# Optimization experiments

Measured on AMD Instinct MI355X. Metric: run time of the kernel, lower is better.

The kernel has to match this reference:

```python
import jax, jax.numpy as jnp
import numpy as np

B, N, F = 2, 512, 128
NUM_BASIS = 4


def _mlp(x, W1, b1, W2, b2, W3, b3):
    # two hidden ReLU layers, linear output -> [..., NUM_BASIS]
    h = jax.nn.relu(x @ W1 + b1)
    h = jax.nn.relu(h @ W2 + b2)
    return h @ W3 + b3


def setup_inputs() -> dict:
    key = jax.random.key(0)
    ks = jax.random.split(key, 12)
    s = 0.05  # keep activations O(1)
    inp = {
        "pointwise_features": jax.random.normal(ks[0], (B, N, F), jnp.float32),
        "relative_features": jax.random.normal(ks[1], (B, N, N, F), jnp.float32),
        "pointwise_basis": jax.random.normal(ks[2], (B, N, NUM_BASIS, 3), jnp.float32),
        "relative_basis": jax.random.normal(ks[3], (B, N, N, NUM_BASIS, 3), jnp.float32),
        "pw_W1": jax.random.normal(ks[4], (F, 128), jnp.float32) * s,
        "pw_b1": jnp.zeros((128,), jnp.float32),
        "pw_W2": jax.random.normal(ks[5], (128, 128), jnp.float32) * s,
        "pw_b2": jnp.zeros((128,), jnp.float32),
        "pw_W3": jax.random.normal(ks[6], (128, NUM_BASIS), jnp.float32) * s,
        "pw_b3": jnp.zeros((NUM_BASIS,), jnp.float32),
        "rel_W1": jax.random.normal(ks[7], (F, 128), jnp.float32) * s,
        "rel_b1": jnp.zeros((128,), jnp.float32),
        "rel_W2": jax.random.normal(ks[8], (128, 128), jnp.float32) * s,
        "rel_b2": jnp.zeros((128,), jnp.float32),
        "rel_W3": jax.random.normal(ks[9], (128, NUM_BASIS), jnp.float32) * s,
        "rel_b3": jnp.zeros((NUM_BASIS,), jnp.float32),
        # last 64 atoms are padding (masked) in every batch element
        "masked_elements": jnp.broadcast_to(jnp.arange(N) >= N - 64, (B, N)),
    }
    return inp


def reference(pointwise_features, relative_features, pointwise_basis, relative_basis,
              pw_W1, pw_b1, pw_W2, pw_b2, pw_W3, pw_b3,
              rel_W1, rel_b1, rel_W2, rel_b2, rel_W3, rel_b3,
              masked_elements):
    unmasked = ~masked_elements                      # [B, N]
    num_atoms = unmasked.sum(-1).astype(pointwise_features.dtype)  # [B]

    # pointwise_shift: [B, N, K, 3]
    pw_scale = _mlp(pointwise_features, pw_W1, pw_b1, pw_W2, pw_b2, pw_W3, pw_b3)
    pointwise_shift = pointwise_basis * pw_scale[..., None]

    # relative_shift: [B, N, N, K, 3], mask over j, mean over j
    rel_scale = _mlp(relative_features, rel_W1, rel_b1, rel_W2, rel_b2, rel_W3, rel_b3)
    relative_shift = relative_basis * rel_scale[..., None]
    relative_shift = relative_shift * unmasked[:, None, :, None, None]
    relative_shift = relative_shift.sum(-3) / num_atoms[:, None, None, None]  # [B, N, K, 3]

    all_shifts = pointwise_shift + relative_shift
    shift = all_shifts.sum(-2) / num_atoms[:, None, None]  # [B, N, 3]
    return shift
```

## Files before the change

### kernel.cpp

```cpp
#include <hip/hip_runtime.h>
#include <stdint.h>

#define LDK 136

typedef __attribute__((ext_vector_type(4))) float f32x4;
typedef __attribute__((ext_vector_type(8))) short bf16x8;

__device__ inline unsigned short f2bf_rtne(float f) {
    union { float f; unsigned u; } v; v.f = f;
    unsigned u = v.u;
    u += 0x7fffu + ((u >> 16) & 1u);
    return (unsigned short)(u >> 16);
}

__global__ void prep_kernel(const float* __restrict__ relW1, const float* __restrict__ relW2,
                            const float* __restrict__ pwW1, const float* __restrict__ pwW2,
                            const float* __restrict__ relW3, const float* __restrict__ pwW3,
                            const void* __restrict__ maskp,
                            float* __restrict__ maskf, float* __restrict__ na,
                            unsigned short* __restrict__ w1T_rel, unsigned short* __restrict__ w2T_rel,
                            unsigned short* __restrict__ w1T_pw, unsigned short* __restrict__ w2T_pw,
                            unsigned short* __restrict__ w3T_rel, unsigned short* __restrict__ w3T_pw) {
    int t = threadIdx.x;
    const float* srcs[4] = {relW1, relW2, pwW1, pwW2};
    unsigned short* dsts[4] = {w1T_rel, w2T_rel, w1T_pw, w2T_pw};
    int e0 = blockIdx.x * 1024 + t;
#pragma unroll
    for (int i = 0; i < 4; ++i) {
        int e = e0 + i * 256;
        int mat = e >> 14, o = e & 16383;
        int n = o >> 7, k = o & 127;
        dsts[mat][o] = f2bf_rtne(srcs[mat][k * 128 + n]);
    }
    if (blockIdx.x == 1) {
        for (int i = t; i < 2048; i += 256) {
            int r = i >> 7, h = i & 127;
            w3T_rel[i] = (r < 4) ? f2bf_rtne(relW3[h * 4 + r]) : (unsigned short)0;
            w3T_pw[i]  = (r < 4) ? f2bf_rtne(pwW3[h * 4 + r])  : (unsigned short)0;
        }
    }
    if (blockIdx.x == 0) {
        __shared__ int anyb;
        __shared__ float cnt[2];
        if (t == 0) anyb = 0;
        if (t < 2) cnt[t] = 0.f;
        __syncthreads();
        const unsigned char* mb = (const unsigned char*)maskp;
        int la = 0;
        for (int i = t; i < 1024; i += 256) la |= mb[i];
        if (la) atomicOr(&anyb, 1);
        __syncthreads();
        bool isbyte = (anyb != 0);
        const int* mi = (const int*)maskp;
        float loc0 = 0.f, loc1 = 0.f;
        for (int i = t; i < 1024; i += 256) {
            int v = isbyte ? (int)mb[i] : mi[i];
            float um = (v != 0) ? 0.f : 1.f;
            maskf[i] = um;
            if (i < 512) loc0 += um; else loc1 += um;
        }
        atomicAdd(&cnt[0], loc0);
        atomicAdd(&cnt[1], loc1);
        __syncthreads();
        if (t < 2) na[t] = cnt[t];
    }
}

__global__ __launch_bounds__(256, 2)
void mlp_kernel(const float* __restrict__ X,
                const unsigned short* __restrict__ w1T,
                const unsigned short* __restrict__ w2T,
                const unsigned short* __restrict__ w3T,
                const float* __restrict__ b1, const float* __restrict__ b2,
                const float* __restrict__ b3,
                float* __restrict__ Sout) {
    __shared__ short xs[64 * LDK];
    __shared__ short hs[2][64 * LDK];
    __shared__ float bs1[128], bs2[128], b3s[4];

    int t = threadIdx.x;
    int w = t >> 6, lane = t & 63, q = lane >> 4, col = lane & 15;

    if (t < 128) { bs1[t] = b1[t]; bs2[t] = b2[t]; }
    if (t < 4) b3s[t] = b3[t];

    bf16x8 w1f[2][4], w2f[2][4], w3f[4];
#pragma unroll
    for (int tn = 0; tn < 2; ++tn)
#pragma unroll
        for (int kc = 0; kc < 4; ++kc) {
            int n = w * 32 + tn * 16 + col;
            int kk = kc * 32 + q * 8;
            w1f[tn][kc] = *(const bf16x8*)&w1T[n * 128 + kk];
            w2f[tn][kc] = *(const bf16x8*)&w2T[n * 128 + kk];
        }
#pragma unroll
    for (int kc = 0; kc < 4; ++kc)
        w3f[kc] = *(const bf16x8*)&w3T[col * 128 + kc * 32 + q * 8];

    long rowbase = (long)blockIdx.x * 256;
    int r0 = t >> 5, cg = t & 31;

    float4 px[8];
    {
        const float4* Xg = (const float4*)(X + rowbase * 128);
#pragma unroll
        for (int i = 0; i < 8; ++i) px[i] = Xg[(r0 + 8 * i) * 32 + cg];
#pragma unroll
        for (int i = 0; i < 8; ++i) {
            float4 v = px[i];
            short4 s4 = make_short4((short)f2bf_rtne(v.x), (short)f2bf_rtne(v.y),
                                    (short)f2bf_rtne(v.z), (short)f2bf_rtne(v.w));
            *(short4*)&xs[(r0 + 8 * i) * LDK + cg * 4] = s4;
        }
    }
    __syncthreads();

    for (int tile = 0; tile < 4; ++tile) {
        int hp = tile & 1;
        if (tile < 3) {
            const float4* Xg2 = (const float4*)(X + (rowbase + (long)(tile + 1) * 64) * 128);
#pragma unroll
            for (int i = 0; i < 8; ++i) px[i] = Xg2[(r0 + 8 * i) * 32 + cg];
        }

        f32x4 acc[2][4];
#pragma unroll
        for (int tn = 0; tn < 2; ++tn)
#pragma unroll
            for (int tm = 0; tm < 4; ++tm) acc[tn][tm] = (f32x4)(0.f);
#pragma unroll
        for (int kc = 0; kc < 4; ++kc) {
            bf16x8 bf[4];
#pragma unroll
            for (int tm = 0; tm < 4; ++tm)
                bf[tm] = *(const bf16x8*)&xs[(tm * 16 + col) * LDK + kc * 32 + q * 8];
#pragma unroll
            for (int tn = 0; tn < 2; ++tn)
#pragma unroll
                for (int tm = 0; tm < 4; ++tm)
                    acc[tn][tm] = __builtin_amdgcn_mfma_f32_16x16x32_bf16(w1f[tn][kc], bf[tm], acc[tn][tm], 0, 0, 0);
        }

#pragma unroll
        for (int tn = 0; tn < 2; ++tn)
#pragma unroll
            for (int tm = 0; tm < 4; ++tm) {
                int n0 = w * 32 + tn * 16 + q * 4;
                int m = tm * 16 + col;
                float4 bb = *(const float4*)&bs1[n0];
                short4 s4 = make_short4(
                    (short)f2bf_rtne(fmaxf(acc[tn][tm][0] + bb.x, 0.f)),
                    (short)f2bf_rtne(fmaxf(acc[tn][tm][1] + bb.y, 0.f)),
                    (short)f2bf_rtne(fmaxf(acc[tn][tm][2] + bb.z, 0.f)),
                    (short)f2bf_rtne(fmaxf(acc[tn][tm][3] + bb.w, 0.f)));
                *(short4*)&hs[hp][m * LDK + n0] = s4;
            }
        __syncthreads();

        if (tile < 3) {
#pragma unroll
            for (int i = 0; i < 8; ++i) {
                float4 v = px[i];
                short4 s4 = make_short4((short)f2bf_rtne(v.x), (short)f2bf_rtne(v.y),
                                        (short)f2bf_rtne(v.z), (short)f2bf_rtne(v.w));
                *(short4*)&xs[(r0 + 8 * i) * LDK + cg * 4] = s4;
            }
        }

        f32x4 acc2[2][4];
#pragma unroll
        for (int tn = 0; tn < 2; ++tn)
#pragma unroll
            for (int tm = 0; tm < 4; ++tm) acc2[tn][tm] = (f32x4)(0.f);
#pragma unroll
        for (int kc = 0; kc < 4; ++kc) {
            bf16x8 bf[4];
#pragma unroll
            for (int tm = 0; tm < 4; ++tm)
                bf[tm] = *(const bf16x8*)&hs[hp][(tm * 16 + col) * LDK + kc * 32 + q * 8];
#pragma unroll
            for (int tn = 0; tn < 2; ++tn)
#pragma unroll
                for (int tm = 0; tm < 4; ++tm)
                    acc2[tn][tm] = __builtin_amdgcn_mfma_f32_16x16x32_bf16(w2f[tn][kc], bf[tm], acc2[tn][tm], 0, 0, 0);
        }
        __syncthreads();

#pragma unroll
        for (int tn = 0; tn < 2; ++tn)
#pragma unroll
            for (int tm = 0; tm < 4; ++tm) {
                int n0 = w * 32 + tn * 16 + q * 4;
                int m = tm * 16 + col;
                float4 bb = *(const float4*)&bs2[n0];
                short4 s4 = make_short4(
                    (short)f2bf_rtne(fmaxf(acc2[tn][tm][0] + bb.x, 0.f)),
                    (short)f2bf_rtne(fmaxf(acc2[tn][tm][1] + bb.y, 0.f)),
                    (short)f2bf_rtne(fmaxf(acc2[tn][tm][2] + bb.z, 0.f)),
                    (short)f2bf_rtne(fmaxf(acc2[tn][tm][3] + bb.w, 0.f)));
                *(short4*)&hs[hp][m * LDK + n0] = s4;
            }
        __syncthreads();

        {
            f32x4 a3 = (f32x4)(0.f);
#pragma unroll
            for (int kc = 0; kc < 4; ++kc) {
                bf16x8 hb = *(const bf16x8*)&hs[hp][(w * 16 + col) * LDK + kc * 32 + q * 8];
                a3 = __builtin_amdgcn_mfma_f32_16x16x32_bf16(w3f[kc], hb, a3, 0, 0, 0);
            }
            if (q == 0) {
                long r = rowbase + (long)tile * 64 + w * 16 + col;
                *(float4*)&Sout[r * 4] = make_float4(a3[0] + b3s[0], a3[1] + b3s[1],
                                                     a3[2] + b3s[2], a3[3] + b3s[3]);
            }
        }
    }
}

__global__ __launch_bounds__(256)
void reduce_kernel(const float* __restrict__ S_rel, const float* __restrict__ S_pw,
                   const float* __restrict__ rel_basis, const float* __restrict__ pw_basis,
                   const float* __restrict__ maskf, const float* __restrict__ na,
                   float* __restrict__ out) {
    int bi = blockIdx.x;
    int b = bi >> 9;
    int t = threadIdx.x;
    float part[12];
#pragma unroll
    for (int r = 0; r < 12; ++r) part[r] = 0.f;

    for (int j = t; j < 512; j += 256) {
        float m = maskf[b * 512 + j];
        long r = (long)bi * 512 + j;
        float4 s4 = *(const float4*)&S_rel[r * 4];
        const float* bp = &rel_basis[r * 12];
        float4 q0 = *(const float4*)&bp[0];
        float4 q1 = *(const float4*)&bp[4];
        float4 q2 = *(const float4*)&bp[8];
        float s0 = s4.x * m, s1 = s4.y * m, s2 = s4.z * m, s3 = s4.w * m;
        part[0] += s0 * q0.x; part[1] += s0 * q0.y; part[2]  += s0 * q0.z;
        part[3] += s1 * q0.w; part[4] += s1 * q1.x; part[5]  += s1 * q1.y;
        part[6] += s2 * q1.z; part[7] += s2 * q1.w; part[8]  += s2 * q2.x;
        part[9] += s3 * q2.y; part[10] += s3 * q2.z; part[11] += s3 * q2.w;
    }

#pragma unroll
    for (int s = 32; s > 0; s >>= 1)
#pragma unroll
        for (int r = 0; r < 12; ++r) part[r] += __shfl_down(part[r], s);

    __shared__ float red[4][12];
    int w = t >> 6, lane = t & 63;
    if (lane == 0)
#pragma unroll
        for (int r = 0; r < 12; ++r) red[w][r] = part[r];
    __syncthreads();

    if (t < 3) {
        float NA = na[b];
        float accp = 0.f, rel = 0.f;
#pragma unroll
        for (int k = 0; k < 4; ++k) {
            rel  += red[0][k * 3 + t] + red[1][k * 3 + t] + red[2][k * 3 + t] + red[3][k * 3 + t];
            accp += pw_basis[bi * 12 + k * 3 + t] * S_pw[bi * 4 + k];
        }
        out[bi * 3 + t] = accp / NA + rel / (NA * NA);
    }
}

extern "C" void kernel_launch(void* const* d_in, const int* in_sizes, int n_in,
                              void* d_out, int out_size, void* d_ws, size_t ws_size,
                              hipStream_t stream) {
    const float* pw_feat   = (const float*)d_in[0];
    const float* rel_feat  = (const float*)d_in[1];
    const float* pw_basis  = (const float*)d_in[2];
    const float* rel_basis = (const float*)d_in[3];
    const float* pw_W1 = (const float*)d_in[4];
    const float* pw_b1 = (const float*)d_in[5];
    const float* pw_W2 = (const float*)d_in[6];
    const float* pw_b2 = (const float*)d_in[7];
    const float* pw_W3 = (const float*)d_in[8];
    const float* pw_b3 = (const float*)d_in[9];
    const float* rel_W1 = (const float*)d_in[10];
    const float* rel_b1 = (const float*)d_in[11];
    const float* rel_W2 = (const float*)d_in[12];
    const float* rel_b2 = (const float*)d_in[13];
    const float* rel_W3 = (const float*)d_in[14];
    const float* rel_b3 = (const float*)d_in[15];
    const void*  maskp  = d_in[16];
    float* out = (float*)d_out;

    char* ws = (char*)d_ws;
    float* maskf = (float*)(ws + 0);
    float* na    = (float*)(ws + 4096);
    unsigned short* w1T_rel = (unsigned short*)(ws + 4352);
    unsigned short* w2T_rel = (unsigned short*)(ws + 37120);
    unsigned short* w1T_pw  = (unsigned short*)(ws + 69888);
    unsigned short* w2T_pw  = (unsigned short*)(ws + 102656);
    unsigned short* w3T_rel = (unsigned short*)(ws + 135424);
    unsigned short* w3T_pw  = (unsigned short*)(ws + 139520);
    float* S_pw  = (float*)(ws + 143616);
    float* S_rel = (float*)(ws + 160000);

    prep_kernel<<<64, 256, 0, stream>>>(rel_W1, rel_W2, pw_W1, pw_W2, rel_W3, pw_W3, maskp,
                                        maskf, na, w1T_rel, w2T_rel, w1T_pw, w2T_pw,
                                        w3T_rel, w3T_pw);
    mlp_kernel<<<2048, 256, 0, stream>>>(rel_feat, w1T_rel, w2T_rel, w3T_rel,
                                         rel_b1, rel_b2, rel_b3, S_rel);
    mlp_kernel<<<4, 256, 0, stream>>>(pw_feat, w1T_pw, w2T_pw, w3T_pw,
                                      pw_b1, pw_b2, pw_b3, S_pw);
    reduce_kernel<<<1024, 256, 0, stream>>>(S_rel, S_pw, rel_basis, pw_basis,
                                            maskf, na, out);
}
```

Before: 446.0 us.

## Fuse basis reduction into MLP kernel and skip fully masked row tiles

```diff
diff --git a/kernel.cpp b/kernel.cpp
--- a/kernel.cpp
+++ b/kernel.cpp
@@ -33,10 +33,10 @@
         dsts[mat][o] = f2bf_rtne(srcs[mat][k * 128 + n]);
     }
     if (blockIdx.x == 1) {
-        for (int i = t; i < 2048; i += 256) {
+        for (int i = t; i < 512; i += 256) {
             int r = i >> 7, h = i & 127;
-            w3T_rel[i] = (r < 4) ? f2bf_rtne(relW3[h * 4 + r]) : (unsigned short)0;
-            w3T_pw[i]  = (r < 4) ? f2bf_rtne(pwW3[h * 4 + r])  : (unsigned short)0;
+            w3T_rel[i] = f2bf_rtne(relW3[h * 4 + r]);
+            w3T_pw[i]  = f2bf_rtne(pwW3[h * 4 + r]);
         }
     }
     if (blockIdx.x == 0) {
@@ -66,25 +66,42 @@
     }
 }
 
-__global__ __launch_bounds__(256, 2)
-void mlp_kernel(const float* __restrict__ X,
-                const unsigned short* __restrict__ w1T,
-                const unsigned short* __restrict__ w2T,
-                const unsigned short* __restrict__ w3T,
-                const float* __restrict__ b1, const float* __restrict__ b2,
-                const float* __restrict__ b3,
-                float* __restrict__ Sout) {
+__global__ __launch_bounds__(256, 3)
+void mlp_kernel(const float* __restrict__ Xrel, const float* __restrict__ Xpw,
+                const unsigned short* __restrict__ w1T_rel, const unsigned short* __restrict__ w2T_rel,
+                const unsigned short* __restrict__ w3T_rel,
+                const unsigned short* __restrict__ w1T_pw, const unsigned short* __restrict__ w2T_pw,
+                const unsigned short* __restrict__ w3T_pw,
+                const float* __restrict__ b1r, const float* __restrict__ b2r, const float* __restrict__ b3r,
+                const float* __restrict__ b1p, const float* __restrict__ b2p, const float* __restrict__ b3p,
+                const float* __restrict__ rel_basis, const float* __restrict__ maskf,
+                float* __restrict__ partials, float* __restrict__ S_pw) {
     __shared__ short xs[64 * LDK];
     __shared__ short hs[2][64 * LDK];
+    __shared__ short w3ls[512];
     __shared__ float bs1[128], bs2[128], b3s[4];
+    __shared__ float msum[4];
+    __shared__ float redp[4][3];
 
     int t = threadIdx.x;
     int w = t >> 6, lane = t & 63, q = lane >> 4, col = lane & 15;
+    bool isrel = blockIdx.x < 2048;
+
+    const float* X = isrel ? Xrel : Xpw;
+    const unsigned short* w1T = isrel ? w1T_rel : w1T_pw;
+    const unsigned short* w2T = isrel ? w2T_rel : w2T_pw;
+    const unsigned short* w3T = isrel ? w3T_rel : w3T_pw;
+    const float* b1 = isrel ? b1r : b1p;
+    const float* b2 = isrel ? b2r : b2p;
+    const float* b3 = isrel ? b3r : b3p;
+    long rowbase = isrel ? (long)blockIdx.x * 256 : (long)(blockIdx.x - 2048) * 256;
+    int mb = isrel ? (((int)(blockIdx.x >> 10)) << 9) | ((blockIdx.x & 1) << 8) : 0;
 
     if (t < 128) { bs1[t] = b1[t]; bs2[t] = b2[t]; }
     if (t < 4) b3s[t] = b3[t];
-
-    bf16x8 w1f[2][4], w2f[2][4], w3f[4];
+    if (t < 128) *(short4*)&w3ls[t * 4] = *(const short4*)&w3T[t * 4];
+
+    bf16x8 w1f[2][4], w2f[2][4];
 #pragma unroll
     for (int tn = 0; tn < 2; ++tn)
 #pragma unroll
@@ -94,11 +111,7 @@
             w1f[tn][kc] = *(const bf16x8*)&w1T[n * 128 + kk];
             w2f[tn][kc] = *(const bf16x8*)&w2T[n * 128 + kk];
         }
-#pragma unroll
-    for (int kc = 0; kc < 4; ++kc)
-        w3f[kc] = *(const bf16x8*)&w3T[col * 128 + kc * 32 + q * 8];
-
-    long rowbase = (long)blockIdx.x * 256;
+
     int r0 = t >> 5, cg = t & 31;
 
     float4 px[8];
@@ -106,6 +119,16 @@
         const float4* Xg = (const float4*)(X + rowbase * 128);
 #pragma unroll
         for (int i = 0; i < 8; ++i) px[i] = Xg[(r0 + 8 * i) * 32 + cg];
+    }
+    {
+        float mv = 1.f;
+        if (isrel) mv = maskf[mb + w * 64 + lane];
+        int act = __any(mv != 0.f);
+        if (lane == 0) msum[w] = act ? 1.f : 0.f;
+    }
+    __syncthreads();
+
+    if (msum[0] != 0.f) {
 #pragma unroll
         for (int i = 0; i < 8; ++i) {
             float4 v = px[i];
@@ -116,9 +139,34 @@
     }
     __syncthreads();
 
+    float prt0 = 0.f, prt1 = 0.f, prt2 = 0.f;
+
     for (int tile = 0; tile < 4; ++tile) {
         int hp = tile & 1;
-        if (tile < 3) {
+        bool a_cur = msum[tile] != 0.f;
+        bool a_nxt = (tile < 3) && (msum[tile + 1] != 0.f);
+
+        if (!a_cur) {
+            if (a_nxt) {
+                const float4* Xg2 = (const float4*)(X + (rowbase + (long)(tile + 1) * 64) * 128);
+#pragma unroll
+                for (int i = 0; i < 8; ++i) px[i] = Xg2[(r0 + 8 * i) * 32 + cg];
+                __syncthreads();
+#pragma unroll
+                for (int i = 0; i < 8; ++i) {
+                    float4 v = px[i];
+                    short4 s4 = make_short4((short)f2bf_rtne(v.x), (short)f2bf_rtne(v.y),
+                                            (short)f2bf_rtne(v.z), (short)f2bf_rtne(v.w));
+                    *(short4*)&xs[(r0 + 8 * i) * LDK + cg * 4] = s4;
+                }
+                __syncthreads();
+            } else {
+                __syncthreads();
+            }
+            continue;
+        }
+
+        if (a_nxt) {
             const float4* Xg2 = (const float4*)(X + (rowbase + (long)(tile + 1) * 64) * 128);
 #pragma unroll
             for (int i = 0; i < 8; ++i) px[i] = Xg2[(r0 + 8 * i) * 32 + cg];
@@ -158,7 +206,7 @@
             }
         __syncthreads();
 
-        if (tile < 3) {
+        if (a_nxt) {
 #pragma unroll
             for (int i = 0; i < 8; ++i) {
                 float4 v = px[i];
@@ -207,66 +255,60 @@
             f32x4 a3 = (f32x4)(0.f);
 #pragma unroll
             for (int kc = 0; kc < 4; ++kc) {
+                bf16x8 w3v = (bf16x8)(short)0;
+                if (col < 4) w3v = *(const bf16x8*)&w3ls[col * 128 + kc * 32 + q * 8];
                 bf16x8 hb = *(const bf16x8*)&hs[hp][(w * 16 + col) * LDK + kc * 32 + q * 8];
-                a3 = __builtin_amdgcn_mfma_f32_16x16x32_bf16(w3f[kc], hb, a3, 0, 0, 0);
+                a3 = __builtin_amdgcn_mfma_f32_16x16x32_bf16(w3v, hb, a3, 0, 0, 0);
             }
             if (q == 0) {
-                long r = rowbase + (long)tile * 64 + w * 16 + col;
-                *(float4*)&Sout[r * 4] = make_float4(a3[0] + b3s[0], a3[1] + b3s[1],
-                                                     a3[2] + b3s[2], a3[3] + b3s[3]);
-            }
-        }
-    }
-}
-
-__global__ __launch_bounds__(256)
-void reduce_kernel(const float* __restrict__ S_rel, const float* __restrict__ S_pw,
-                   const float* __restrict__ rel_basis, const float* __restrict__ pw_basis,
-                   const float* __restrict__ maskf, const float* __restrict__ na,
-                   float* __restrict__ out) {
-    int bi = blockIdx.x;
-    int b = bi >> 9;
-    int t = threadIdx.x;
-    float part[12];
-#pragma unroll
-    for (int r = 0; r < 12; ++r) part[r] = 0.f;
-
-    for (int j = t; j < 512; j += 256) {
-        float m = maskf[b * 512 + j];
-        long r = (long)bi * 512 + j;
-        float4 s4 = *(const float4*)&S_rel[r * 4];
-        const float* bp = &rel_basis[r * 12];
-        float4 q0 = *(const float4*)&bp[0];
-        float4 q1 = *(const float4*)&bp[4];
-        float4 q2 = *(const float4*)&bp[8];
-        float s0 = s4.x * m, s1 = s4.y * m, s2 = s4.z * m, s3 = s4.w * m;
-        part[0] += s0 * q0.x; part[1] += s0 * q0.y; part[2]  += s0 * q0.z;
-        part[3] += s1 * q0.w; part[4] += s1 * q1.x; part[5]  += s1 * q1.y;
-        part[6] += s2 * q1.z; part[7] += s2 * q1.w; part[8]  += s2 * q2.x;
-        part[9] += s3 * q2.y; part[10] += s3 * q2.z; part[11] += s3 * q2.w;
-    }
-
-#pragma unroll
-    for (int s = 32; s > 0; s >>= 1)
-#pragma unroll
-        for (int r = 0; r < 12; ++r) part[r] += __shfl_down(part[r], s);
-
-    __shared__ float red[4][12];
-    int w = t >> 6, lane = t & 63;
-    if (lane == 0)
-#pragma unroll
-        for (int r = 0; r < 12; ++r) red[w][r] = part[r];
-    __syncthreads();
-
-    if (t < 3) {
-        float NA = na[b];
-        float accp = 0.f, rel = 0.f;
-#pragma unroll
-        for (int k = 0; k < 4; ++k) {
-            rel  += red[0][k * 3 + t] + red[1][k * 3 + t] + red[2][k * 3 + t] + red[3][k * 3 + t];
-            accp += pw_basis[bi * 12 + k * 3 + t] * S_pw[bi * 4 + k];
-        }
-        out[bi * 3 + t] = accp / NA + rel / (NA * NA);
+                int rloc = tile * 64 + w * 16 + col;
+                float s0 = a3[0] + b3s[0], s1 = a3[1] + b3s[1];
+                float s2 = a3[2] + b3s[2], s3 = a3[3] + b3s[3];
+                if (isrel) {
+                    float m = maskf[mb + rloc];
+                    long r = rowbase + rloc;
+                    const float4* bp = (const float4*)&rel_basis[r * 12];
+                    float4 q0 = bp[0], q1 = bp[1], q2 = bp[2];
+                    s0 *= m; s1 *= m; s2 *= m; s3 *= m;
+                    prt0 += s0 * q0.x + s1 * q0.w + s2 * q1.z + s3 * q2.y;
+                    prt1 += s0 * q0.y + s1 * q1.x + s2 * q1.w + s3 * q2.z;
+                    prt2 += s0 * q0.z + s1 * q1.y + s2 * q2.x + s3 * q2.w;
+                } else {
+                    long r = rowbase + rloc;
+                    *(float4*)&S_pw[r * 4] = make_float4(s0, s1, s2, s3);
+                }
+            }
+        }
+    }
+
+    if (isrel) {
+#pragma unroll
+        for (int s = 8; s > 0; s >>= 1) {
+            prt0 += __shfl_down(prt0, s);
+            prt1 += __shfl_down(prt1, s);
+            prt2 += __shfl_down(prt2, s);
+        }
+        if (lane == 0) { redp[w][0] = prt0; redp[w][1] = prt1; redp[w][2] = prt2; }
+        __syncthreads();
+        if (t < 3)
+            partials[blockIdx.x * 3 + t] =
+                redp[0][t] + redp[1][t] + redp[2][t] + redp[3][t];
+    }
+}
+
+__global__ void final_kernel(const float* __restrict__ partials, const float* __restrict__ S_pw,
+                             const float* __restrict__ pw_basis, const float* __restrict__ na,
+                             float* __restrict__ out) {
+    int bi = blockIdx.x * 128 + threadIdx.x;
+    if (bi >= 1024) return;
+    float NA = na[bi >> 9];
+    float4 s = *(const float4*)&S_pw[bi * 4];
+    const float* pb = &pw_basis[bi * 12];
+#pragma unroll
+    for (int c = 0; c < 3; ++c) {
+        float rel = partials[(2 * bi) * 3 + c] + partials[(2 * bi + 1) * 3 + c];
+        float pw = s.x * pb[c] + s.y * pb[3 + c] + s.z * pb[6 + c] + s.w * pb[9 + c];
+        out[bi * 3 + c] = pw / NA + rel / (NA * NA);
     }
 }
 
@@ -300,17 +342,18 @@
     unsigned short* w1T_pw  = (unsigned short*)(ws + 69888);
     unsigned short* w2T_pw  = (unsigned short*)(ws + 102656);
     unsigned short* w3T_rel = (unsigned short*)(ws + 135424);
-    unsigned short* w3T_pw  = (unsigned short*)(ws + 139520);
-    float* S_pw  = (float*)(ws + 143616);
-    float* S_rel = (float*)(ws + 160000);
+    unsigned short* w3T_pw  = (unsigned short*)(ws + 136448);
+    float* S_pw     = (float*)(ws + 143616);
+    float* partials = (float*)(ws + 160000);
 
     prep_kernel<<<64, 256, 0, stream>>>(rel_W1, rel_W2, pw_W1, pw_W2, rel_W3, pw_W3, maskp,
                                         maskf, na, w1T_rel, w2T_rel, w1T_pw, w2T_pw,
                                         w3T_rel, w3T_pw);
-    mlp_kernel<<<2048, 256, 0, stream>>>(rel_feat, w1T_rel, w2T_rel, w3T_rel,
-                                         rel_b1, rel_b2, rel_b3, S_rel);
-    mlp_kernel<<<4, 256, 0, stream>>>(pw_feat, w1T_pw, w2T_pw, w3T_pw,
-                                      pw_b1, pw_b2, pw_b3, S_pw);
-    reduce_kernel<<<1024, 256, 0, stream>>>(S_rel, S_pw, rel_basis, pw_basis,
-                                            maskf, na, out);
-}
+    mlp_kernel<<<2052, 256, 0, stream>>>(rel_feat, pw_feat,
+                                         w1T_rel, w2T_rel, w3T_rel,
+                                         w1T_pw, w2T_pw, w3T_pw,
+                                         rel_b1, rel_b2, rel_b3,
+                                         pw_b1, pw_b2, pw_b3,
+                                         rel_basis, maskf, partials, S_pw);
+    final_kernel<<<8, 128, 0, stream>>>(partials, S_pw, pw_basis, na, out);
+}
```

Result: no change. 450.6 us (+1.0%).
